# Optimization experiments

Measured on AMD Instinct MI355X. Metric: run time of the kernel, lower is better.

The kernel has to match this reference:

```python
import jax, jax.numpy as jnp
import numpy as np
from jax import lax


def setup_inputs() -> dict:
    key = jax.random.key(0)
    k1, k2, k3 = jax.random.split(key, 3)
    B, T, D, K = 64, 512, 1024, 32
    x = jax.random.normal(k1, (B, T, D), dtype=jnp.float32)
    W = jax.random.normal(k2, (D, K), dtype=jnp.float32) * (1.0 / np.sqrt(D))
    U = jax.random.normal(k3, (K, K), dtype=jnp.float32) * 0.1
    b = jnp.zeros((K,), dtype=jnp.float32)
    return {"x": x, "W": W, "U": U, "b": b}


def _crf_marginals(x, W, U, b):
    # Emission (input) energies: linear activation of x @ W + b -> [B, T, K]
    e = jnp.einsum('btd,dk->btk', x, W) + b
    e_t = jnp.swapaxes(e, 0, 1)  # [T, B, K]

    # Forward recursion: alpha_t = logsumexp_prev(alpha_{t-1} + U) + e_t
    def fwd_step(alpha, et):
        a = jax.nn.logsumexp(alpha[:, :, None] + U[None, :, :], axis=1) + et
        return a, a

    alpha0 = e_t[0]
    _, alphas = lax.scan(fwd_step, alpha0, e_t[1:])
    alpha = jnp.concatenate([alpha0[None], alphas], axis=0)  # [T, B, K]

    # Backward recursion: beta_t = logsumexp_next(U + e_{t+1} + beta_{t+1})
    def bwd_step(beta, et_next):
        nb = jax.nn.logsumexp(U[None, :, :] + (et_next + beta)[:, None, :], axis=2)
        return nb, nb

    betaT = jnp.zeros_like(alpha0)
    _, betas = lax.scan(bwd_step, betaT, e_t[1:], reverse=True)
    beta = jnp.concatenate([betas, betaT[None]], axis=0)  # [T, B, K]

    # Marginal probability of each tag at each timestep
    marg = jax.nn.softmax(alpha + beta, axis=-1)  # [T, B, K]
    return jnp.swapaxes(marg, 0, 1)  # [B, T, K]


def reference(x, W, U, b):
    return _crf_marginals(x, W, U, b)
```

## Files before the change

kernel.cpp:

```cpp
#include <hip/hip_runtime.h>

#define TT 512
#define BB 64
#define DD 1024
#define KK 32

__device__ __forceinline__ float rfl(float v) {
  return __int_as_float(__builtin_amdgcn_readfirstlane(__float_as_int(v)));
}

__global__ __launch_bounds__(256) void emit_kernel(
    const float* __restrict__ x, const float* __restrict__ W,
    const float* __restrict__ bias, float* __restrict__ F) {
  __shared__ float4 Ls4[2048];
  const int t = threadIdx.x;
  const int l = t & 63;
  const int w = t >> 6;
  const int rg = l >> 2;
  const int kg = l & 3;
  const int m0 = blockIdx.x * 64;
  const int r0 = m0 + rg * 4;

  const float* xp0 = x + (size_t)r0 * DD + w * 256;
  const float* xp1 = xp0 + DD;
  const float* xp2 = xp1 + DD;
  const float* xp3 = xp2 + DD;

  float acc[4][8];
#pragma unroll
  for (int j = 0; j < 4; ++j)
#pragma unroll
    for (int k = 0; k < 8; ++k) acc[j][k] = 0.f;

  float4 xa0 = *(const float4*)(xp0);
  float4 xa1 = *(const float4*)(xp1);
  float4 xa2 = *(const float4*)(xp2);
  float4 xa3 = *(const float4*)(xp3);

#pragma unroll 1
  for (int c = 0; c < 4; ++c) {
    const float4* Wg4 = (const float4*)(W + (size_t)(w * 256 + c * 64) * KK);
    float4 pw[8];
#pragma unroll
    for (int i = 0; i < 8; ++i) pw[i] = Wg4[i * 64 + l];
#pragma unroll
    for (int i = 0; i < 8; ++i) Ls4[w * 512 + i * 64 + l] = pw[i];

#pragma unroll
    for (int gg = 0; gg < 16; ++gg) {
      const int dd = c * 64 + gg * 4;
      int nd = dd + 4; if (nd > 252) nd = 252;
      float4 xb0 = *(const float4*)(xp0 + nd);
      float4 xb1 = *(const float4*)(xp1 + nd);
      float4 xb2 = *(const float4*)(xp2 + nd);
      float4 xb3 = *(const float4*)(xp3 + nd);
#pragma unroll
      for (int d2 = 0; d2 < 4; ++d2) {
        const int wb = w * 512 + (gg * 4 + d2) * 8 + kg * 2;
        float4 wlo = Ls4[wb];
        float4 whi = Ls4[wb + 1];
        const float x0 = ((const float*)&xa0)[d2];
        const float x1 = ((const float*)&xa1)[d2];
        const float x2 = ((const float*)&xa2)[d2];
        const float x3 = ((const float*)&xa3)[d2];
        acc[0][0]=fmaf(x0,wlo.x,acc[0][0]); acc[0][1]=fmaf(x0,wlo.y,acc[0][1]);
        acc[0][2]=fmaf(x0,wlo.z,acc[0][2]); acc[0][3]=fmaf(x0,wlo.w,acc[0][3]);
        acc[0][4]=fmaf(x0,whi.x,acc[0][4]); acc[0][5]=fmaf(x0,whi.y,acc[0][5]);
        acc[0][6]=fmaf(x0,whi.z,acc[0][6]); acc[0][7]=fmaf(x0,whi.w,acc[0][7]);
        acc[1][0]=fmaf(x1,wlo.x,acc[1][0]); acc[1][1]=fmaf(x1,wlo.y,acc[1][1]);
        acc[1][2]=fmaf(x1,wlo.z,acc[1][2]); acc[1][3]=fmaf(x1,wlo.w,acc[1][3]);
        acc[1][4]=fmaf(x1,whi.x,acc[1][4]); acc[1][5]=fmaf(x1,whi.y,acc[1][5]);
        acc[1][6]=fmaf(x1,whi.z,acc[1][6]); acc[1][7]=fmaf(x1,whi.w,acc[1][7]);
        acc[2][0]=fmaf(x2,wlo.x,acc[2][0]); acc[2][1]=fmaf(x2,wlo.y,acc[2][1]);
        acc[2][2]=fmaf(x2,wlo.z,acc[2][2]); acc[2][3]=fmaf(x2,wlo.w,acc[2][3]);
        acc[2][4]=fmaf(x2,whi.x,acc[2][4]); acc[2][5]=fmaf(x2,whi.y,acc[2][5]);
        acc[2][6]=fmaf(x2,whi.z,acc[2][6]); acc[2][7]=fmaf(x2,whi.w,acc[2][7]);
        acc[3][0]=fmaf(x3,wlo.x,acc[3][0]); acc[3][1]=fmaf(x3,wlo.y,acc[3][1]);
        acc[3][2]=fmaf(x3,wlo.z,acc[3][2]); acc[3][3]=fmaf(x3,wlo.w,acc[3][3]);
        acc[3][4]=fmaf(x3,whi.x,acc[3][4]); acc[3][5]=fmaf(x3,whi.y,acc[3][5]);
        acc[3][6]=fmaf(x3,whi.z,acc[3][6]); acc[3][7]=fmaf(x3,whi.w,acc[3][7]);
      }
      xa0 = xb0; xa1 = xb1; xa2 = xb2; xa3 = xb3;
    }
  }

  __syncthreads();
#pragma unroll
  for (int j = 0; j < 4; ++j) {
    Ls4[w * 512 + (rg * 4 + j) * 8 + kg * 2] =
        make_float4(acc[j][0], acc[j][1], acc[j][2], acc[j][3]);
    Ls4[w * 512 + (rg * 4 + j) * 8 + kg * 2 + 1] =
        make_float4(acc[j][4], acc[j][5], acc[j][6], acc[j][7]);
  }
  __syncthreads();
  const int rr = t >> 2;
  const int kc = t & 3;
  float4 s0 = Ls4[rr * 8 + kc * 2];
  float4 s1 = Ls4[rr * 8 + kc * 2 + 1];
#pragma unroll
  for (int q2 = 1; q2 < 4; ++q2) {
    float4 a0 = Ls4[q2 * 512 + rr * 8 + kc * 2];
    float4 a1 = Ls4[q2 * 512 + rr * 8 + kc * 2 + 1];
    s0.x += a0.x; s0.y += a0.y; s0.z += a0.z; s0.w += a0.w;
    s1.x += a1.x; s1.y += a1.y; s1.z += a1.z; s1.w += a1.w;
  }
  float4 bv0 = *(const float4*)(bias + kc * 8);
  float4 bv1 = *(const float4*)(bias + kc * 8 + 4);
  float4 e0, e1;
  e0.x = __expf(s0.x + bv0.x); e0.y = __expf(s0.y + bv0.y);
  e0.z = __expf(s0.z + bv0.z); e0.w = __expf(s0.w + bv0.w);
  e1.x = __expf(s1.x + bv1.x); e1.y = __expf(s1.y + bv1.y);
  e1.z = __expf(s1.z + bv1.z); e1.w = __expf(s1.w + bv1.w);
  float4* F4 = (float4*)(F + (size_t)(m0 + rr) * KK);
  F4[kc * 2] = e0;
  F4[kc * 2 + 1] = e1;
}

__global__ __launch_bounds__(64) void scan_kernel(
    const float* __restrict__ F, const float* __restrict__ U,
    float* __restrict__ A, float* __restrict__ Bw) {
  __shared__ __align__(16) float cur[KK];
  const int l = threadIdx.x;
  const int kk = l & 31;
  const int h = l >> 5;
  const int seg = blockIdx.x & 15;
  const int b = (blockIdx.x >> 4) & 63;
  const int dir = blockIdx.x >> 10;

  const float* Fb = F + (size_t)b * TT * KK;
  float V[16];

  if (dir == 0) {
    float* Ab = A + (size_t)b * TT * KK;
#pragma unroll
    for (int j = 0; j < 16; ++j) V[j] = __expf(U[(h * 16 + j) * KK + kk]);
    const int lo = seg * 32, hi = seg * 32 + 31;
    const int t0 = (seg == 0) ? 0 : lo - 17;
    float a = Fb[t0 * KK + kk];
    cur[kk] = a;
    if (seg == 0 && l < 32) Ab[l] = a;
    __builtin_amdgcn_wave_barrier();

#define FSTEP(fv, tcur)                                                     \
    {                                                                       \
      const float4* c4 = (const float4*)cur;                                \
      float4 y0 = c4[h*4+0], y1 = c4[h*4+1], y2 = c4[h*4+2], y3 = c4[h*4+3];\
      float r = __builtin_amdgcn_rcpf(rfl(y0.x));                           \
      float s0 = fmaf(y0.x, V[0],  fmaf(y0.y, V[1],                         \
                 fmaf(y0.z, V[2],  y0.w * V[3])));                          \
      float s1 = fmaf(y1.x, V[4],  fmaf(y1.y, V[5],                         \
                 fmaf(y1.z, V[6],  y1.w * V[7])));                          \
      float s2 = fmaf(y2.x, V[8],  fmaf(y2.y, V[9],                         \
                 fmaf(y2.z, V[10], y2.w * V[11])));                         \
      float s3 = fmaf(y3.x, V[12], fmaf(y3.y, V[13],                        \
                 fmaf(y3.z, V[14], y3.w * V[15])));                         \
      float s = (s0 + s1) + (s2 + s3);                                      \
      s += __shfl_xor(s, 32);                                               \
      a = s * ((fv) * r);                                                   \
      cur[kk] = a;                                                          \
      __builtin_amdgcn_wave_barrier();                                      \
      if ((tcur) >= lo && l < 32) Ab[(tcur) * KK + l] = a;                  \
    }

    int t = t0 + 1;
    float f0 = Fb[t * KK + kk],       f1 = Fb[(t + 1) * KK + kk];
    float f2 = Fb[(t + 2) * KK + kk], f3 = Fb[(t + 3) * KK + kk];
    for (; t + 3 <= hi; t += 4) {
      int tn = t + 4;
      int u0 = tn     > hi ? hi : tn;
      int u1 = tn + 1 > hi ? hi : tn + 1;
      int u2 = tn + 2 > hi ? hi : tn + 2;
      int u3 = tn + 3 > hi ? hi : tn + 3;
      float n0 = Fb[u0 * KK + kk], n1 = Fb[u1 * KK + kk];
      float n2 = Fb[u2 * KK + kk], n3 = Fb[u3 * KK + kk];
      FSTEP(f0, t); FSTEP(f1, t + 1); FSTEP(f2, t + 2); FSTEP(f3, t + 3);
      f0 = n0; f1 = n1; f2 = n2; f3 = n3;
    }
    if (t <= hi) { FSTEP(f0, t); ++t; }
    if (t <= hi) { FSTEP(f1, t); ++t; }
    if (t <= hi) { FSTEP(f2, t); ++t; }
#undef FSTEP
  } else {
    const int b2 = b;
    float* Bb = Bw + (size_t)b2 * TT * KK;
#pragma unroll
    for (int j = 0; j < 16; ++j) V[j] = __expf(U[kk * KK + h * 16 + j]);
    const int lo = seg * 32;
    const int hs = seg * 32 + 31;
    const int t1 = (seg == 15) ? (TT - 1) : (lo + 48);
    float g = Fb[t1 * KK + kk];
    cur[kk] = g;
    if (seg == 15 && l < 32) Bb[(TT - 1) * KK + l] = 1.0f;
    __builtin_amdgcn_wave_barrier();

#define BSTEP(fv, tcur)                                                     \
    {                                                                       \
      const float4* c4 = (const float4*)cur;                                \
      float4 y0 = c4[h*4+0], y1 = c4[h*4+1], y2 = c4[h*4+2], y3 = c4[h*4+3];\
      float r = __builtin_amdgcn_rcpf(rfl(y0.x));                           \
      float s0 = fmaf(y0.x, V[0],  fmaf(y0.y, V[1],                         \
                 fmaf(y0.z, V[2],  y0.w * V[3])));                          \
      float s1 = fmaf(y1.x, V[4],  fmaf(y1.y, V[5],                         \
                 fmaf(y1.z, V[6],  y1.w * V[7])));                          \
      float s2 = fmaf(y2.x, V[8],  fmaf(y2.y, V[9],                         \
                 fmaf(y2.z, V[10], y2.w * V[11])));                         \
      float s3 = fmaf(y3.x, V[12], fmaf(y3.y, V[13],                        \
                 fmaf(y3.z, V[14], y3.w * V[15])));                         \
      float s = (s0 + s1) + (s2 + s3);                                      \
      s += __shfl_xor(s, 48);                                               \
      s = (s0 + s1) + (s2 + s3) == s ? s : s;              \
      float bnew = s * r;                                                   \
      g = bnew * (fv);                                                      \
      cur[kk] = g;                                                          \
      __builtin_amdgcn_wave_barrier();                                      \
      if ((tcur) <= hs && l < 32) Bb[(tcur) * KK + l] = bnew;               \
    }
#undef BSTEP
#define BSTEP(fv, tcur)                                                     \
    {                                                                       \
      const float4* c4 = (const float4*)cur;                                \
      float4 y0 = c4[h*4+0], y1 = c4[h*4+1], y2 = c4[h*4+2], y3 = c4[h*4+3];\
      float r = __builtin_amdgcn_rcpf(rfl(y0.x));                           \
      float s0 = fmaf(y0.x, V[0],  fmaf(y0.y, V[1],                         \
                 fmaf(y0.z, V[2],  y0.w * V[3])));                          \
      float s1 = fmaf(y1.x, V[4],  fmaf(y1.y, V[5],                         \
                 fmaf(y1.z, V[6],  y1.w * V[7])));                          \
      float s2 = fmaf(y2.x, V[8],  fmaf(y2.y, V[9],                         \
                 fmaf(y2.z, V[10], y2.w * V[11])));                         \
      float s3 = fmaf(y3.x, V[12], fmaf(y3.y, V[13],                        \
                 fmaf(y3.z, V[14], y3.w * V[15])));                         \
      float s = (s0 + s1) + (s2 + s3);                                      \
      s += __shfl_xor(s, 32);                                               \
      float bnew = s * r;                                                   \
      g = bnew * (fv);                                                      \
      cur[kk] = g;                                                          \
      __builtin_amdgcn_wave_barrier();                                      \
      if ((tcur) <= hs && l < 32) Bb[(tcur) * KK + l] = bnew;               \
    }

    int t = t1 - 1;
    float f0 = Fb[t * KK + kk],       f1 = Fb[(t - 1) * KK + kk];
    float f2 = Fb[(t - 2) * KK + kk], f3 = Fb[(t - 3) * KK + kk];
    for (; t - 3 >= lo; t -= 4) {
      int tn = t - 4;
      int u0 = tn     < 0 ? 0 : tn;
      int u1 = tn - 1 < 0 ? 0 : tn - 1;
      int u2 = tn - 2 < 0 ? 0 : tn - 2;
      int u3 = tn - 3 < 0 ? 0 : tn - 3;
      float n0 = Fb[u0 * KK + kk], n1 = Fb[u1 * KK + kk];
      float n2 = Fb[u2 * KK + kk], n3 = Fb[u3 * KK + kk];
      BSTEP(f0, t); BSTEP(f1, t - 1); BSTEP(f2, t - 2); BSTEP(f3, t - 3);
      f0 = n0; f1 = n1; f2 = n2; f3 = n3;
    }
    if (t >= lo) { BSTEP(f0, t); --t; }
    if (t >= lo) { BSTEP(f1, t); --t; }
    if (t >= lo) { BSTEP(f2, t); --t; }
#undef BSTEP
  }
}

__global__ __launch_bounds__(256) void combine_kernel(
    const float* __restrict__ Bw, float* __restrict__ out) {
  size_t i = (size_t)blockIdx.x * 256 + threadIdx.x;
  float p = out[i] * Bw[i];
  float ssum = p;
  ssum += __shfl_xor(ssum, 1);
  ssum += __shfl_xor(ssum, 2);
  ssum += __shfl_xor(ssum, 4);
  ssum += __shfl_xor(ssum, 8);
  ssum += __shfl_xor(ssum, 16);
  out[i] = p / ssum;
}

extern "C" void kernel_launch(void* const* d_in, const int* in_sizes, int n_in,
                              void* d_out, int out_size, void* d_ws, size_t ws_size,
                              hipStream_t stream) {
  const float* x = (const float*)d_in[0];
  const float* W = (const float*)d_in[1];
  const float* U = (const float*)d_in[2];
  const float* b = (const float*)d_in[3];
  float* out = (float*)d_out;
  float* F = (float*)d_ws;
  float* Bw = F + (size_t)BB * TT * KK;

  emit_kernel<<<512, 256, 0, stream>>>(x, W, b, F);
  scan_kernel<<<2048, 64, 0, stream>>>(F, U, out, Bw);
  combine_kernel<<<(BB * TT * KK) / 256, 256, 0, stream>>>(Bw, out);
}
```

Before: 237.6 us.

## Shrink emission GEMM tile to one row per lane and prefetch W chunks

The emission kernel now has each block handle 16 rows instead of 64, each lane accumulating one row times 8 tags. It launches 4x more blocks with half the shared memory and asks for 8 blocks per CU through launch bounds. W chunks are now double-buffered in registers, loading the next 32-row slice while the current one is used. The aim is higher occupancy and more in-flight memory traffic for this bandwidth-bound GEMV-like stage, at the cost of less W reuse per LDS load and more redundant W reads across blocks. A dead, immediately undefined macro is also removed.

```diff
diff --git a/kernel.cpp b/kernel.cpp
--- a/kernel.cpp
+++ b/kernel.cpp
@@ -9,111 +9,82 @@
   return __int_as_float(__builtin_amdgcn_readfirstlane(__float_as_int(v)));
 }
 
-__global__ __launch_bounds__(256) void emit_kernel(
+__global__ __launch_bounds__(256, 8) void emit_kernel(
     const float* __restrict__ x, const float* __restrict__ W,
     const float* __restrict__ bias, float* __restrict__ F) {
-  __shared__ float4 Ls4[2048];
+  __shared__ float4 Ls4[1024];
   const int t = threadIdx.x;
   const int l = t & 63;
   const int w = t >> 6;
   const int rg = l >> 2;
   const int kg = l & 3;
-  const int m0 = blockIdx.x * 64;
-  const int r0 = m0 + rg * 4;
-
-  const float* xp0 = x + (size_t)r0 * DD + w * 256;
-  const float* xp1 = xp0 + DD;
-  const float* xp2 = xp1 + DD;
-  const float* xp3 = xp2 + DD;
-
-  float acc[4][8];
-#pragma unroll
-  for (int j = 0; j < 4; ++j)
-#pragma unroll
-    for (int k = 0; k < 8; ++k) acc[j][k] = 0.f;
-
-  float4 xa0 = *(const float4*)(xp0);
-  float4 xa1 = *(const float4*)(xp1);
-  float4 xa2 = *(const float4*)(xp2);
-  float4 xa3 = *(const float4*)(xp3);
+  const int m0 = blockIdx.x * 16;
+  const int r = m0 + rg;
+
+  const float* xp = x + (size_t)r * DD + w * 256;
+
+  float acc[8];
+#pragma unroll
+  for (int k = 0; k < 8; ++k) acc[k] = 0.f;
+
+  float4 xa = *(const float4*)(xp);
+
+  const float4* Wg4 = (const float4*)(W) + (size_t)w * 2048;
+  float4 pw[4];
+#pragma unroll
+  for (int i = 0; i < 4; ++i) pw[i] = Wg4[i * 64 + l];
 
 #pragma unroll 1
-  for (int c = 0; c < 4; ++c) {
-    const float4* Wg4 = (const float4*)(W + (size_t)(w * 256 + c * 64) * KK);
-    float4 pw[8];
-#pragma unroll
-    for (int i = 0; i < 8; ++i) pw[i] = Wg4[i * 64 + l];
-#pragma unroll
-    for (int i = 0; i < 8; ++i) Ls4[w * 512 + i * 64 + l] = pw[i];
-
-#pragma unroll
-    for (int gg = 0; gg < 16; ++gg) {
-      const int dd = c * 64 + gg * 4;
+  for (int c = 0; c < 8; ++c) {
+#pragma unroll
+    for (int i = 0; i < 4; ++i) Ls4[w * 256 + i * 64 + l] = pw[i];
+
+    if (c < 7) {
+#pragma unroll
+      for (int i = 0; i < 4; ++i) pw[i] = Wg4[(c + 1) * 256 + i * 64 + l];
+    }
+
+#pragma unroll
+    for (int gg = 0; gg < 8; ++gg) {
+      const int dd = c * 32 + gg * 4;
       int nd = dd + 4; if (nd > 252) nd = 252;
-      float4 xb0 = *(const float4*)(xp0 + nd);
-      float4 xb1 = *(const float4*)(xp1 + nd);
-      float4 xb2 = *(const float4*)(xp2 + nd);
-      float4 xb3 = *(const float4*)(xp3 + nd);
+      float4 xb = *(const float4*)(xp + nd);
 #pragma unroll
       for (int d2 = 0; d2 < 4; ++d2) {
-        const int wb = w * 512 + (gg * 4 + d2) * 8 + kg * 2;
+        const int wb = w * 256 + (gg * 4 + d2) * 8 + kg * 2;
         float4 wlo = Ls4[wb];
         float4 whi = Ls4[wb + 1];
-        const float x0 = ((const float*)&xa0)[d2];
-        const float x1 = ((const float*)&xa1)[d2];
-        const float x2 = ((const float*)&xa2)[d2];
-        const float x3 = ((const float*)&xa3)[d2];
-        acc[0][0]=fmaf(x0,wlo.x,acc[0][0]); acc[0][1]=fmaf(x0,wlo.y,acc[0][1]);
-        acc[0][2]=fmaf(x0,wlo.z,acc[0][2]); acc[0][3]=fmaf(x0,wlo.w,acc[0][3]);
-        acc[0][4]=fmaf(x0,whi.x,acc[0][4]); acc[0][5]=fmaf(x0,whi.y,acc[0][5]);
-        acc[0][6]=fmaf(x0,whi.z,acc[0][6]); acc[0][7]=fmaf(x0,whi.w,acc[0][7]);
-        acc[1][0]=fmaf(x1,wlo.x,acc[1][0]); acc[1][1]=fmaf(x1,wlo.y,acc[1][1]);
-        acc[1][2]=fmaf(x1,wlo.z,acc[1][2]); acc[1][3]=fmaf(x1,wlo.w,acc[1][3]);
-        acc[1][4]=fmaf(x1,whi.x,acc[1][4]); acc[1][5]=fmaf(x1,whi.y,acc[1][5]);
-        acc[1][6]=fmaf(x1,whi.z,acc[1][6]); acc[1][7]=fmaf(x1,whi.w,acc[1][7]);
-        acc[2][0]=fmaf(x2,wlo.x,acc[2][0]); acc[2][1]=fmaf(x2,wlo.y,acc[2][1]);
-        acc[2][2]=fmaf(x2,wlo.z,acc[2][2]); acc[2][3]=fmaf(x2,wlo.w,acc[2][3]);
-        acc[2][4]=fmaf(x2,whi.x,acc[2][4]); acc[2][5]=fmaf(x2,whi.y,acc[2][5]);
-        acc[2][6]=fmaf(x2,whi.z,acc[2][6]); acc[2][7]=fmaf(x2,whi.w,acc[2][7]);
-        acc[3][0]=fmaf(x3,wlo.x,acc[3][0]); acc[3][1]=fmaf(x3,wlo.y,acc[3][1]);
-        acc[3][2]=fmaf(x3,wlo.z,acc[3][2]); acc[3][3]=fmaf(x3,wlo.w,acc[3][3]);
-        acc[3][4]=fmaf(x3,whi.x,acc[3][4]); acc[3][5]=fmaf(x3,whi.y,acc[3][5]);
-        acc[3][6]=fmaf(x3,whi.z,acc[3][6]); acc[3][7]=fmaf(x3,whi.w,acc[3][7]);
+        const float x0 = ((const float*)&xa)[d2];
+        acc[0] = fmaf(x0, wlo.x, acc[0]); acc[1] = fmaf(x0, wlo.y, acc[1]);
+        acc[2] = fmaf(x0, wlo.z, acc[2]); acc[3] = fmaf(x0, wlo.w, acc[3]);
+        acc[4] = fmaf(x0, whi.x, acc[4]); acc[5] = fmaf(x0, whi.y, acc[5]);
+        acc[6] = fmaf(x0, whi.z, acc[6]); acc[7] = fmaf(x0, whi.w, acc[7]);
       }
-      xa0 = xb0; xa1 = xb1; xa2 = xb2; xa3 = xb3;
+      xa = xb;
     }
   }
 
   __syncthreads();
-#pragma unroll
-  for (int j = 0; j < 4; ++j) {
-    Ls4[w * 512 + (rg * 4 + j) * 8 + kg * 2] =
-        make_float4(acc[j][0], acc[j][1], acc[j][2], acc[j][3]);
-    Ls4[w * 512 + (rg * 4 + j) * 8 + kg * 2 + 1] =
-        make_float4(acc[j][4], acc[j][5], acc[j][6], acc[j][7]);
+  Ls4[w * 128 + rg * 8 + kg * 2] =
+      make_float4(acc[0], acc[1], acc[2], acc[3]);
+  Ls4[w * 128 + rg * 8 + kg * 2 + 1] =
+      make_float4(acc[4], acc[5], acc[6], acc[7]);
+  __syncthreads();
+  if (t < 128) {
+    const int rr = t >> 3;
+    const int kc = t & 7;
+    float4 s = Ls4[rr * 8 + kc];
+#pragma unroll
+    for (int q = 1; q < 4; ++q) {
+      float4 a = Ls4[q * 128 + rr * 8 + kc];
+      s.x += a.x; s.y += a.y; s.z += a.z; s.w += a.w;
+    }
+    float4 bv = *(const float4*)(bias + kc * 4);
+    float4 e;
+    e.x = __expf(s.x + bv.x); e.y = __expf(s.y + bv.y);
+    e.z = __expf(s.z + bv.z); e.w = __expf(s.w + bv.w);
+    ((float4*)(F + (size_t)(m0 + rr) * KK))[kc] = e;
   }
-  __syncthreads();
-  const int rr = t >> 2;
-  const int kc = t & 3;
-  float4 s0 = Ls4[rr * 8 + kc * 2];
-  float4 s1 = Ls4[rr * 8 + kc * 2 + 1];
-#pragma unroll
-  for (int q2 = 1; q2 < 4; ++q2) {
-    float4 a0 = Ls4[q2 * 512 + rr * 8 + kc * 2];
-    float4 a1 = Ls4[q2 * 512 + rr * 8 + kc * 2 + 1];
-    s0.x += a0.x; s0.y += a0.y; s0.z += a0.z; s0.w += a0.w;
-    s1.x += a1.x; s1.y += a1.y; s1.z += a1.z; s1.w += a1.w;
-  }
-  float4 bv0 = *(const float4*)(bias + kc * 8);
-  float4 bv1 = *(const float4*)(bias + kc * 8 + 4);
-  float4 e0, e1;
-  e0.x = __expf(s0.x + bv0.x); e0.y = __expf(s0.y + bv0.y);
-  e0.z = __expf(s0.z + bv0.z); e0.w = __expf(s0.w + bv0.w);
-  e1.x = __expf(s1.x + bv1.x); e1.y = __expf(s1.y + bv1.y);
-  e1.z = __expf(s1.z + bv1.z); e1.w = __expf(s1.w + bv1.w);
-  float4* F4 = (float4*)(F + (size_t)(m0 + rr) * KK);
-  F4[kc * 2] = e0;
-  F4[kc * 2 + 1] = e1;
 }
 
 __global__ __launch_bounds__(64) void scan_kernel(
@@ -193,29 +164,6 @@
     if (seg == 15 && l < 32) Bb[(TT - 1) * KK + l] = 1.0f;
     __builtin_amdgcn_wave_barrier();
 
-#define BSTEP(fv, tcur)                                                     \
-    {                                                                       \
-      const float4* c4 = (const float4*)cur;                                \
-      float4 y0 = c4[h*4+0], y1 = c4[h*4+1], y2 = c4[h*4+2], y3 = c4[h*4+3];\
-      float r = __builtin_amdgcn_rcpf(rfl(y0.x));                           \
-      float s0 = fmaf(y0.x, V[0],  fmaf(y0.y, V[1],                         \
-                 fmaf(y0.z, V[2],  y0.w * V[3])));                          \
-      float s1 = fmaf(y1.x, V[4],  fmaf(y1.y, V[5],                         \
-                 fmaf(y1.z, V[6],  y1.w * V[7])));                          \
-      float s2 = fmaf(y2.x, V[8],  fmaf(y2.y, V[9],                         \
-                 fmaf(y2.z, V[10], y2.w * V[11])));                         \
-      float s3 = fmaf(y3.x, V[12], fmaf(y3.y, V[13],                        \
-                 fmaf(y3.z, V[14], y3.w * V[15])));                         \
-      float s = (s0 + s1) + (s2 + s3);                                      \
-      s += __shfl_xor(s, 48);                                               \
-      s = (s0 + s1) + (s2 + s3) == s ? s : s;              \
-      float bnew = s * r;                                                   \
-      g = bnew * (fv);                                                      \
-      cur[kk] = g;                                                          \
-      __builtin_amdgcn_wave_barrier();                                      \
-      if ((tcur) <= hs && l < 32) Bb[(tcur) * KK + l] = bnew;               \
-    }
-#undef BSTEP
 #define BSTEP(fv, tcur)                                                     \
     {                                                                       \
       const float4* c4 = (const float4*)cur;                                \
@@ -283,7 +231,7 @@
   float* F = (float*)d_ws;
   float* Bw = F + (size_t)BB * TT * KK;
 
-  emit_kernel<<<512, 256, 0, stream>>>(x, W, b, F);
+  emit_kernel<<<2048, 256, 0, stream>>>(x, W, b, F);
   scan_kernel<<<2048, 64, 0, stream>>>(F, U, out, Bw);
   combine_kernel<<<(BB * TT * KK) / 256, 256, 0, stream>>>(Bw, out);
 }
```

After: 309.2 us. 1.3x slower.
